# Optimization experiments

Measured on AMD Instinct MI355X. Metric: run time of the kernel, lower is better.

Reference implementation:

```python
import jax, jax.numpy as jnp
import numpy as np

N = 27          # number of graph nodes (hardcoded in the module)
NH = 28         # n_hidden = out_features = self_size + 1
H = 8192        # n_heads
HA = 256        # num_hiddens_action
NO = 5          # num_outputs_action


def setup_inputs() -> dict:
    key = jax.random.key(0)
    ks = jax.random.split(key, 8)
    # node_embeddings: one_hot(node, 27) ++ reward flag (reward_nodes=[2] -> node index 1)
    node_emb = jnp.concatenate(
        [jnp.eye(N, dtype=jnp.float32),
         (jnp.arange(N) == 1).astype(jnp.float32)[:, None]], axis=1)  # [27,28]
    # adjacency [27,27,1], 0/1 ints, self-loops forced so softmax columns are valid
    adj = (jax.random.uniform(ks[0], (N, N, 1)) < 0.3).astype(jnp.int32)
    adj = adj.at[jnp.arange(N), jnp.arange(N), 0].set(1)
    # obs: one-hot current-location vector, node index 5 -> cur_node = 6
    obs = jnp.zeros((1, N), dtype=jnp.float32).at[0, 5].set(1.0)
    s = 0.02
    W_lin = jax.random.normal(ks[1], (N + 1, NH * H), dtype=jnp.float32) * s
    W_attn = jax.random.normal(ks[2], (2 * NH, 1), dtype=jnp.float32) * s
    b_attn = jax.random.normal(ks[3], (1,), dtype=jnp.float32) * s
    W1 = jax.random.normal(ks[4], (N + 1, HA), dtype=jnp.float32) * s
    b1 = jax.random.normal(ks[5], (HA,), dtype=jnp.float32) * s
    W2 = jax.random.normal(ks[6], (HA, NO), dtype=jnp.float32) * s
    b2 = jax.random.normal(ks[7], (NO,), dtype=jnp.float32) * s
    return {"obs": obs, "node_emb": node_emb, "adj": adj, "W_lin": W_lin,
            "W_attn": W_attn, "b_attn": b_attn, "W1": W1, "b1": b1,
            "W2": W2, "b2": b2}


def _leaky(x, slope):
    return jnp.where(x >= 0, x, slope * x)


def reference(obs, node_emb, adj, W_lin, W_attn, b_attn, W1, b1, W2, b2):
    # per-head projection: [27,28] @ [28, 28*8192] -> [27, H, NH]
    g = (node_emb @ W_lin).reshape(N, H, NH)
    # attn(concat(g_i, g_j)) decomposed: e[i,j,h] = g_i.Wl + g_j.Wr + b
    # (mathematically identical to the repeat/repeat_interleave + concat path,
    #  avoids materializing the [27,27,H,2*NH] tensor)
    Wl = W_attn[:NH, 0]
    Wr = W_attn[NH:, 0]
    s_i = jnp.einsum('nhf,f->nh', g, Wl)  # [N,H]
    s_j = jnp.einsum('nhf,f->nh', g, Wr)  # [N,H]
    e = _leaky(s_i[:, None, :] + s_j[None, :, :] + b_attn[0], 0.2)  # [N,N,H]
    # mask non-edges; adj [N,N,1] broadcasts over heads
    e = jnp.where(adj == 0, -jnp.inf, e)
    # torch nn.Softmax() with no dim resolves to dim=0 for 3-D input
    a = jax.nn.softmax(e, axis=0)
    # dropout is identity in eval mode
    attn_res = jnp.einsum('ijh,jhf->ihf', a, g)  # [N,H,NH]
    attn_res = attn_res.mean(axis=1)             # is_concat=False -> [N,NH]
    # cur_node = get_loc(bool obs) + 1; select attn_res[cur_node-1]
    idx = jnp.argmax(obs[0] != 0)
    x = attn_res[idx]                            # [NH]
    h = _leaky(x @ W1 + b1, 0.01)                # default LeakyReLU slope
    return h @ W2 + b2                           # [NO]
```

## Files before the change

### kernel.cpp

```cpp
#include <hip/hip_runtime.h>
#include <math.h>

#define NN 27
#define KD 28
#define HD 8192
#define HA_ 256
#define NO_ 5
#define NPAIR (KD*HD)
#define HB 8
#define NBLK (HD/HB)


__global__ void __launch_bounds__(256, 4) kMain(const float* __restrict__ obs,
                                                const int* __restrict__ adj,
                                                const float* __restrict__ Wlin,
                                                const float* __restrict__ Wattn,
                                                const float* __restrict__ battn,
                                                float* __restrict__ ws) {
    __shared__ float P[HB][KD + 1];
    __shared__ float Q[HB][KD + 1];
    __shared__ float A[HB][KD];
    __shared__ unsigned adjm[NN];
    __shared__ float red[4][KD];

    const int t  = threadIdx.x;
    const int k  = t >> 3;
    const int hl = t & 7;
    const int h  = blockIdx.x * HB + hl;

    if (t < NN) {
        unsigned m = 0;
        for (int i = 0; i < NN; ++i) m |= (adj[i * NN + t] != 0 ? 1u : 0u) << i;
        adjm[t] = m;
    }

    float4 wv[7];
    if (k < KD) {
        const float4* src = reinterpret_cast<const float4*>(
            Wlin + (size_t)k * NPAIR + (size_t)h * KD);
        const float4* wl4 = reinterpret_cast<const float4*>(Wattn);
        const float4* wr4 = reinterpret_cast<const float4*>(Wattn + KD);
#pragma unroll
        for (int f4 = 0; f4 < 7; ++f4) wv[f4] = src[f4];
        float p = 0.f, q = 0.f;
#pragma unroll
        for (int f4 = 0; f4 < 7; ++f4) {
            float4 wl = wl4[f4], wr = wr4[f4], w = wv[f4];
            p += w.x * wl.x + w.y * wl.y + w.z * wl.z + w.w * wl.w;
            q += w.x * wr.x + w.y * wr.y + w.z * wr.z + w.w * wr.w;
        }
        P[hl][k] = p;
        Q[hl][k] = q;
    }
    __syncthreads();

    if (t < HB * NN) {
        const int hl2 = t / NN, j = t - hl2 * NN;
        int idx = 0;
        for (int n = NN - 1; n >= 0; --n) if (obs[n] != 0.f) idx = n;
        const float bias = battn[0];
        const float p27 = P[hl2][27], q27 = Q[hl2][27];
        const float sj = Q[hl2][j] + (j == 1 ? q27 : 0.f) + bias;
        const unsigned msk = adjm[j];
        float mx = -3.0e38f;
#pragma unroll
        for (int i = 0; i < NN; ++i) {
            float e = P[hl2][i] + (i == 1 ? p27 : 0.f) + sj;
            e = e >= 0.f ? e : 0.2f * e;
            if (((msk >> i) & 1) && e > mx) mx = e;
        }
        float den = 0.f, num = 0.f;
#pragma unroll
        for (int i = 0; i < NN; ++i) {
            float e = P[hl2][i] + (i == 1 ? p27 : 0.f) + sj;
            e = e >= 0.f ? e : 0.2f * e;
            float x = ((msk >> i) & 1) ? __expf(e - mx) : 0.f;
            den += x;
            if (i == idx) num = x;
        }
        A[hl2][j] = num / den;
    }
    __syncthreads();

    float acc[KD];
    if (k < KD) {
        const float bk = A[hl][k < NN ? k : 1];
#pragma unroll
        for (int f4 = 0; f4 < 7; ++f4) {
            acc[4*f4+0] = bk * wv[f4].x;
            acc[4*f4+1] = bk * wv[f4].y;
            acc[4*f4+2] = bk * wv[f4].z;
            acc[4*f4+3] = bk * wv[f4].w;
        }
    } else {
#pragma unroll
        for (int f = 0; f < KD; ++f) acc[f] = 0.f;
    }
#pragma unroll
    for (int off = 32; off > 0; off >>= 1)
#pragma unroll
        for (int f = 0; f < KD; ++f) acc[f] += __shfl_xor(acc[f], off, 64);

    const int lane = t & 63, wv_id = t >> 6;
    if (lane == 0) {
#pragma unroll
        for (int f = 0; f < KD; ++f) red[wv_id][f] = acc[f];
    }
    __syncthreads();
    if (t < KD)
        ws[blockIdx.x * KD + t] = red[0][t] + red[1][t] + red[2][t] + red[3][t];
}

__global__ void __launch_bounds__(512) kF(const float* __restrict__ W1,
                                          const float* __restrict__ b1,
                                          const float* __restrict__ W2,
                                          const float* __restrict__ b2,
                                          const float* __restrict__ ws,
                                          float* __restrict__ out) {
    __shared__ float xp[KD][16];
    __shared__ float x[KD];
    __shared__ float hh[HA_];
    const int t = threadIdx.x;
    if (t < 16 * KD) {
        const int seg = t / KD, f = t - seg * KD;
        float s = 0.f;
#pragma unroll 4
        for (int b = seg; b < NBLK; b += 16) s += ws[b * KD + f];
        xp[f][seg] = s;
    }
    __syncthreads();
    if (t < KD) {
        float s = 0.f;
#pragma unroll
        for (int g = 0; g < 16; ++g) s += xp[t][g];
        x[t] = s * (1.0f / HD);
    }
    __syncthreads();
    if (t < HA_) {
        float s = b1[t];
#pragma unroll
        for (int kk = 0; kk < KD; ++kk) s += x[kk] * W1[kk * HA_ + t];
        hh[t] = s >= 0.f ? s : 0.01f * s;
    }
    __syncthreads();
    if (t < NO_) {
        float s = b2[t];
        for (int u = 0; u < HA_; ++u) s += hh[u] * W2[u * NO_ + t];
        out[t] = s;
    }
}

extern "C" void kernel_launch(void* const* d_in, const int* in_sizes, int n_in,
                              void* d_out, int out_size, void* d_ws, size_t ws_size,
                              hipStream_t stream) {
    const float* obs   = (const float*)d_in[0];
    const int*   adj   = (const int*)  d_in[2];
    const float* Wlin  = (const float*)d_in[3];
    const float* Wattn = (const float*)d_in[4];
    const float* battn = (const float*)d_in[5];
    const float* W1    = (const float*)d_in[6];
    const float* b1    = (const float*)d_in[7];
    const float* W2    = (const float*)d_in[8];
    const float* b2    = (const float*)d_in[9];
    float* ws  = (float*)d_ws;
    float* out = (float*)d_out;

    kMain<<<NBLK, 256, 0, stream>>>(obs, adj, Wlin, Wattn, battn, ws);
    kF<<<1, 512, 0, stream>>>(W1, b1, W2, b2, ws, out);
}
```

Before: 30.17 us.

## Fuse final MLP into main kernel via atomic slot reduction and last-block tail

The separate reduction/MLP kernel is removed. Each block atomically adds its partial sums into one of 64 slot buffers, and the last block to finish, found through an atomic counter, reduces the slots and runs the small MLP. This is meant to save the second kernel launch and its serial read of all per-block partials. In exchange it adds a memset launch, atomic contention on the slots, and a non-deterministic float summation order.

```diff
diff --git a/kernel.cpp b/kernel.cpp
--- a/kernel.cpp
+++ b/kernel.cpp
@@ -9,19 +9,26 @@
 #define NPAIR (KD*HD)
 #define HB 8
 #define NBLK (HD/HB)
+#define SLOTS 64
 
 
-__global__ void __launch_bounds__(256, 4) kMain(const float* __restrict__ obs,
-                                                const int* __restrict__ adj,
-                                                const float* __restrict__ Wlin,
-                                                const float* __restrict__ Wattn,
-                                                const float* __restrict__ battn,
-                                                float* __restrict__ ws) {
+__global__ void __launch_bounds__(256, 4) kFused(const float* __restrict__ obs,
+                                                 const int* __restrict__ adj,
+                                                 const float* __restrict__ Wlin,
+                                                 const float* __restrict__ Wattn,
+                                                 const float* __restrict__ battn,
+                                                 const float* __restrict__ W1,
+                                                 const float* __restrict__ b1,
+                                                 const float* __restrict__ W2,
+                                                 const float* __restrict__ b2,
+                                                 float* __restrict__ ws,
+                                                 float* __restrict__ out) {
     __shared__ float P[HB][KD + 1];
     __shared__ float Q[HB][KD + 1];
     __shared__ float A[HB][KD];
     __shared__ unsigned adjm[NN];
     __shared__ float red[4][KD];
+    __shared__ int isLast;
 
     const int t  = threadIdx.x;
     const int k  = t >> 3;
@@ -107,46 +114,43 @@
         for (int f = 0; f < KD; ++f) red[wv_id][f] = acc[f];
     }
     __syncthreads();
-    if (t < KD)
-        ws[blockIdx.x * KD + t] = red[0][t] + red[1][t] + red[2][t] + red[3][t];
-}
-
-__global__ void __launch_bounds__(512) kF(const float* __restrict__ W1,
-                                          const float* __restrict__ b1,
-                                          const float* __restrict__ W2,
-                                          const float* __restrict__ b2,
-                                          const float* __restrict__ ws,
-                                          float* __restrict__ out) {
-    __shared__ float xp[KD][16];
-    __shared__ float x[KD];
-    __shared__ float hh[HA_];
-    const int t = threadIdx.x;
-    if (t < 16 * KD) {
-        const int seg = t / KD, f = t - seg * KD;
-        float s = 0.f;
-#pragma unroll 4
-        for (int b = seg; b < NBLK; b += 16) s += ws[b * KD + f];
-        xp[f][seg] = s;
+    if (t < KD) {
+        float partial = red[0][t] + red[1][t] + red[2][t] + red[3][t];
+        atomicAdd(&ws[(blockIdx.x & (SLOTS - 1)) * KD + t], partial);
     }
     __syncthreads();
-    if (t < KD) {
-        float s = 0.f;
-#pragma unroll
-        for (int g = 0; g < 16; ++g) s += xp[t][g];
-        x[t] = s * (1.0f / HD);
+    if (t == 0) {
+        __threadfence();
+        int* counter = (int*)(ws + SLOTS * KD);
+        int old = atomicAdd(counter, 1);
+        isLast = (old == NBLK - 1);
     }
     __syncthreads();
-    if (t < HA_) {
-        float s = b1[t];
+
+    if (isLast) {
+        __shared__ float x[KD];
+        __shared__ float hh[HA_];
+        if (t < KD) {
+            float s = 0.f;
+#pragma unroll 8
+            for (int sl = 0; sl < SLOTS; ++sl)
+                s += __hip_atomic_load(&ws[sl * KD + t], __ATOMIC_RELAXED,
+                                       __HIP_MEMORY_SCOPE_AGENT);
+            x[t] = s * (1.0f / HD);
+        }
+        __syncthreads();
+        if (t < HA_) {
+            float s = b1[t];
 #pragma unroll
-        for (int kk = 0; kk < KD; ++kk) s += x[kk] * W1[kk * HA_ + t];
-        hh[t] = s >= 0.f ? s : 0.01f * s;
-    }
-    __syncthreads();
-    if (t < NO_) {
-        float s = b2[t];
-        for (int u = 0; u < HA_; ++u) s += hh[u] * W2[u * NO_ + t];
-        out[t] = s;
+            for (int kk = 0; kk < KD; ++kk) s += x[kk] * W1[kk * HA_ + t];
+            hh[t] = s >= 0.f ? s : 0.01f * s;
+        }
+        __syncthreads();
+        if (t < NO_) {
+            float s = b2[t];
+            for (int u = 0; u < HA_; ++u) s += hh[u] * W2[u * NO_ + t];
+            out[t] = s;
+        }
     }
 }
 
@@ -165,6 +169,7 @@
     float* ws  = (float*)d_ws;
     float* out = (float*)d_out;
 
-    kMain<<<NBLK, 256, 0, stream>>>(obs, adj, Wlin, Wattn, battn, ws);
-    kF<<<1, 512, 0, stream>>>(W1, b1, W2, b2, ws, out);
+    hipMemsetAsync(ws, 0, SLOTS * KD * sizeof(float) + sizeof(int), stream);
+    kFused<<<NBLK, 256, 0, stream>>>(obs, adj, Wlin, Wattn, battn,
+                                     W1, b1, W2, b2, ws, out);
 }
```

Result: slower. 42.81 us (+41.9%).
